# Kernel optimization log

Measured on AMD Instinct MI355X. Metric: run time of the kernel, lower is better.

## Reference

```python
import jax, jax.numpy as jnp
import numpy as np

B, N, C = 8, 1024, 768
H, D = 12, 64  # num_heads, head_dim
SCALE = D ** -0.5


def setup_inputs() -> dict:
    key = jax.random.key(0)
    ks = jax.random.split(key, 6)
    x = jax.random.normal(ks[0], (B, N, C), dtype=jnp.float32)
    # per-head Linear weights stacked: [H, D, C] (torch Linear stores [out, in])
    Wq = jax.random.normal(ks[1], (H, D, C), dtype=jnp.float32) * 0.02
    Wk = jax.random.normal(ks[2], (H, D, C), dtype=jnp.float32) * 0.02
    Wv = jax.random.normal(ks[3], (H, D, C), dtype=jnp.float32) * 0.02
    Wp = jax.random.normal(ks[4], (C, C), dtype=jnp.float32) * 0.02
    bp = jnp.zeros((C,), dtype=jnp.float32)
    return {"x": x, "Wq": Wq, "Wk": Wk, "Wv": Wv, "Wp": Wp, "bp": bp}


def reference(x, Wq, Wk, Wv, Wp, bp):
    # Per-head projections (batched across heads): [B, H, N, D]
    q = jnp.einsum('bnc,hdc->bhnd', x, Wq) * SCALE
    k = jnp.einsum('bnc,hdc->bhnd', x, Wk)
    v = jnp.einsum('bnc,hdc->bhnd', x, Wv)
    # Scaled dot-product attention per head
    attn = jax.nn.softmax(jnp.einsum('bhnd,bhmd->bhnm', q, k), axis=-1)
    out = jnp.einsum('bhnm,bhmd->bhnd', attn, v)
    # Concat heads along last dim == transpose to [B, N, H, D] then reshape
    out = out.transpose(0, 2, 1, 3).reshape(x.shape[0], x.shape[1], -1)
    # Output projection
    return out @ Wp.T + bp
```

## Files before the change

### kernel.cpp

```cpp
#include <hip/hip_runtime.h>

typedef unsigned short u16;
typedef __attribute__((ext_vector_type(8))) __bf16 bf16x8;
typedef __attribute__((ext_vector_type(4))) float f32x4;

__device__ __forceinline__ u16 f2bf(float f) {
    union { float f; unsigned u; } v; v.f = f;
    unsigned u = v.u;
    u += 0x7FFFu + ((u >> 16) & 1u);
    return (u16)(u >> 16);
}

typedef const __attribute__((address_space(1))) void GV;
typedef __attribute__((address_space(3))) void LV;
__device__ __forceinline__ void gl2lds16(const void* g, void* l) {
    __builtin_amdgcn_global_load_lds((GV*)g, (LV*)l, 16, 0, 0);
}

__global__ void cast_f32_to_bf16(const float* __restrict__ in, u16* __restrict__ out, int n4) {
    int i = blockIdx.x * 256 + threadIdx.x;
    if (i < n4) {
        float4 f = reinterpret_cast<const float4*>(in)[i];
        ushort4 o;
        o.x = f2bf(f.x); o.y = f2bf(f.y); o.z = f2bf(f.z); o.w = f2bf(f.w);
        reinterpret_cast<ushort4*>(out)[i] = o;
    }
}

__device__ __forceinline__ void stage_tile32(const u16* src, int k0, u16* lds, int tid) {
    #pragma unroll
    for (int half = 0; half < 2; half++) {
        int i = half * 256 + tid;
        int row = i >> 2, p = i & 3;
        int l = (p - (row >> 1)) & 3;
        gl2lds16(src + (size_t)row * 768 + k0 + l * 8, lds + i * 8);
    }
}
__device__ __forceinline__ const bf16x8* frag32(const u16* lds, int row, int quad) {
    return reinterpret_cast<const bf16x8*>(lds + row * 32 + (((quad + (row >> 1)) & 3) * 8));
}

__global__ __launch_bounds__(256, 2) void gemm_qkv(
    const u16* __restrict__ A, const u16* __restrict__ Bm,
    u16* __restrict__ qo, u16* __restrict__ ko, u16* __restrict__ vto)
{
    __shared__ u16 As[4096];
    __shared__ u16 Bs[4096];
    const int tid = threadIdx.x;
    const int wave = tid >> 6, lane = tid & 63;
    const int quad = lane >> 4, l16 = lane & 15;
    const int wr = (wave >> 1) * 64, wc = (wave & 1) * 64;
    const int rowBase = blockIdx.y * 128;
    const int colBase = blockIdx.x * 128;

    f32x4 acc[4][4] = {};
    const u16* aSrc = A + (size_t)rowBase * 768;
    const u16* bSrc = Bm + (size_t)colBase * 768;

    for (int k0 = 0; k0 < 768; k0 += 32) {
        __syncthreads();
        stage_tile32(aSrc, k0, As, tid);
        stage_tile32(bSrc, k0, Bs, tid);
        __syncthreads();
        bf16x8 a[4], b[4];
        #pragma unroll
        for (int mi = 0; mi < 4; mi++)
            a[mi] = *frag32(As, wr + mi * 16 + l16, quad);
        #pragma unroll
        for (int ni = 0; ni < 4; ni++)
            b[ni] = *frag32(Bs, wc + ni * 16 + l16, quad);
        #pragma unroll
        for (int mi = 0; mi < 4; mi++)
            #pragma unroll
            for (int ni = 0; ni < 4; ni++)
                acc[mi][ni] = __builtin_amdgcn_mfma_f32_16x16x32_bf16(a[mi], b[ni], acc[mi][ni], 0, 0, 0);
    }

    #pragma unroll
    for (int mi = 0; mi < 4; mi++) {
        #pragma unroll
        for (int ni = 0; ni < 4; ni++) {
            int gj = colBase + wc + ni * 16 + l16;
            int which = gj / 768;
            int r = gj - which * 768;
            int h = r >> 6, d = r & 63;
            int gi0 = rowBase + wr + mi * 16 + quad * 4;
            int b_ = gi0 >> 10;
            int n0 = gi0 & 1023;
            if (which == 2) {
                ushort4 pk;
                pk.x = f2bf(acc[mi][ni][0]);
                pk.y = f2bf(acc[mi][ni][1]);
                pk.z = f2bf(acc[mi][ni][2]);
                pk.w = f2bf(acc[mi][ni][3]);
                *reinterpret_cast<ushort4*>(vto + ((size_t)(b_ * 12 + h) * 64 + d) * 1024 + n0) = pk;
            } else {
                float s = (which == 0) ? 0.125f : 1.0f;
                u16* dst = (which == 0 ? qo : ko) + ((size_t)(b_ * 12 + h) * 1024 + n0) * 64 + d;
                #pragma unroll
                for (int rr = 0; rr < 4; rr++)
                    dst[(size_t)rr * 64] = f2bf(acc[mi][ni][rr] * s);
            }
        }
    }
}

__global__ __launch_bounds__(256, 3) void attn_fwd(
    const u16* __restrict__ q, const u16* __restrict__ k,
    const u16* __restrict__ vt, u16* __restrict__ ao)
{
    __shared__ u16 Ks[2][4096];
    __shared__ u16 Vs[2][4096];
    __shared__ u16 Ps[128][72];
    const int bh = blockIdx.x, qt = blockIdx.y;
    const int b = bh / 12, h = bh - b * 12;
    const int tid = threadIdx.x;
    const int wave = tid >> 6, lane = tid & 63;
    const int quad = lane >> 4, l16 = lane & 15;
    const int swz = l16 & 7;
    u16 (*PsW)[72] = &Ps[wave * 32];

    const u16* qb = q + (size_t)bh * 65536 + ((size_t)qt * 128 + wave * 32) * 64;
    const u16* kb = k + (size_t)bh * 65536;
    const u16* vb = vt + (size_t)bh * 65536;

    auto stage = [&](int buf, int j0) {
        #pragma unroll
        for (int r = 0; r < 2; r++) {
            int i = r * 256 + tid;
            int row = i >> 3, cp = i & 7;
            int cl = cp ^ (row & 7);
            gl2lds16((const char*)kb + (size_t)(j0 + row) * 128 + cl * 16,
                     (char*)&Ks[buf][0] + i * 16);
        }
        #pragma unroll
        for (int r = 0; r < 2; r++) {
            int i = r * 256 + tid;
            int row = i >> 3, cp = i & 7;
            int cl = cp ^ (row & 7);
            gl2lds16((const char*)vb + (size_t)row * 2048 + (size_t)j0 * 2 + cl * 16,
                     (char*)&Vs[buf][0] + i * 16);
        }
    };

    stage(0, 0);

    bf16x8 qf[2][2];
    #pragma unroll
    for (int ni = 0; ni < 2; ni++)
        #pragma unroll
        for (int ks = 0; ks < 2; ks++)
            qf[ni][ks] = *reinterpret_cast<const bf16x8*>(qb + (ni * 16 + l16) * 64 + ks * 32 + quad * 8);

    f32x4 o[2][4] = {};
    float lsum[2] = {0.f, 0.f};

    __syncthreads();

    int buf = 0;
    for (int j0 = 0; j0 < 1024; j0 += 64) {
        if (j0 + 64 < 1024) stage(buf ^ 1, j0 + 64);

        f32x4 s[4][2] = {};
        #pragma unroll
        for (int ks = 0; ks < 2; ks++) {
            bf16x8 kf[4];
            #pragma unroll
            for (int mi = 0; mi < 4; mi++) {
                int row = mi * 16 + l16;
                int ch = (ks * 4 + quad) ^ swz;
                kf[mi] = *reinterpret_cast<const bf16x8*>(&Ks[buf][row * 64 + ch * 8]);
            }
            #pragma unroll
            for (int mi = 0; mi < 4; mi++)
                #pragma unroll
                for (int ni = 0; ni < 2; ni++)
                    s[mi][ni] = __builtin_amdgcn_mfma_f32_16x16x32_bf16(kf[mi], qf[ni][ks], s[mi][ni], 0, 0, 0);
        }

        #pragma unroll
        for (int mi = 0; mi < 4; mi++) {
            #pragma unroll
            for (int ni = 0; ni < 2; ni++) {
                float p0 = __expf(s[mi][ni][0]);
                float p1 = __expf(s[mi][ni][1]);
                float p2 = __expf(s[mi][ni][2]);
                float p3 = __expf(s[mi][ni][3]);
                lsum[ni] += (p0 + p1) + (p2 + p3);
                ushort4 pk;
                pk.x = f2bf(p0); pk.y = f2bf(p1); pk.z = f2bf(p2); pk.w = f2bf(p3);
                *reinterpret_cast<ushort4*>(&PsW[ni * 16 + l16][mi * 16 + quad * 4]) = pk;
            }
        }

        #pragma unroll
        for (int ks = 0; ks < 2; ks++) {
            bf16x8 vf[4], pf[2];
            #pragma unroll
            for (int di = 0; di < 4; di++) {
                int row = di * 16 + l16;
                int ch = (ks * 4 + quad) ^ swz;
                vf[di] = *reinterpret_cast<const bf16x8*>(&Vs[buf][row * 64 + ch * 8]);
            }
            #pragma unroll
            for (int mi = 0; mi < 2; mi++)
                pf[mi] = *reinterpret_cast<const bf16x8*>(&PsW[mi * 16 + l16][ks * 32 + quad * 8]);
            #pragma unroll
            for (int mi = 0; mi < 2; mi++)
                #pragma unroll
                for (int di = 0; di < 4; di++)
                    o[mi][di] = __builtin_amdgcn_mfma_f32_16x16x32_bf16(pf[mi], vf[di], o[mi][di], 0, 0, 0);
        }

        __syncthreads();
        buf ^= 1;
    }

    #pragma unroll
    for (int ni = 0; ni < 2; ni++) {
        lsum[ni] += __shfl_xor(lsum[ni], 16, 64);
        lsum[ni] += __shfl_xor(lsum[ni], 32, 64);
    }

    #pragma unroll
    for (int mi = 0; mi < 2; mi++) {
        #pragma unroll
        for (int r = 0; r < 4; r++) {
            float lv = __shfl(lsum[mi], quad * 4 + r, 16);
            float inv = 1.0f / lv;
            int n = qt * 128 + wave * 32 + mi * 16 + quad * 4 + r;
            size_t base = (size_t)(b * 1024 + n) * 768 + h * 64;
            #pragma unroll
            for (int di = 0; di < 4; di++)
                ao[base + di * 16 + l16] = f2bf(o[mi][di][r] * inv);
        }
    }
}

__global__ __launch_bounds__(256, 2) void gemm_proj(
    const u16* __restrict__ A, const u16* __restrict__ Bm,
    const float* __restrict__ bias, float* __restrict__ out)
{
    __shared__ u16 As[4096];
    __shared__ u16 Bs[4096];
    const int tid = threadIdx.x;
    const int wave = tid >> 6, lane = tid & 63;
    const int quad = lane >> 4, l16 = lane & 15;
    const int wr = (wave >> 1) * 64, wc = (wave & 1) * 64;
    const int rowBase = blockIdx.y * 128;
    const int colBase = blockIdx.x * 128;

    f32x4 acc[4][4] = {};
    const u16* aSrc = A + (size_t)rowBase * 768;
    const u16* bSrc = Bm + (size_t)colBase * 768;

    for (int k0 = 0; k0 < 768; k0 += 32) {
        __syncthreads();
        stage_tile32(aSrc, k0, As, tid);
        stage_tile32(bSrc, k0, Bs, tid);
        __syncthreads();
        bf16x8 a[4], b[4];
        #pragma unroll
        for (int mi = 0; mi < 4; mi++)
            a[mi] = *frag32(As, wr + mi * 16 + l16, quad);
        #pragma unroll
        for (int ni = 0; ni < 4; ni++)
            b[ni] = *frag32(Bs, wc + ni * 16 + l16, quad);
        #pragma unroll
        for (int mi = 0; mi < 4; mi++)
            #pragma unroll
            for (int ni = 0; ni < 4; ni++)
                acc[mi][ni] = __builtin_amdgcn_mfma_f32_16x16x32_bf16(a[mi], b[ni], acc[mi][ni], 0, 0, 0);
    }

    #pragma unroll
    for (int mi = 0; mi < 4; mi++) {
        #pragma unroll
        for (int ni = 0; ni < 4; ni++) {
            int gj = colBase + wc + ni * 16 + l16;
            float bv = bias[gj];
            int gi0 = rowBase + wr + mi * 16 + quad * 4;
            #pragma unroll
            for (int rr2 = 0; rr2 < 4; rr2++)
                out[(size_t)(gi0 + rr2) * 768 + gj] = acc[mi][ni][rr2] + bv;
        }
    }
}

extern "C" void kernel_launch(void* const* d_in, const int* in_sizes, int n_in,
                              void* d_out, int out_size, void* d_ws, size_t ws_size,
                              hipStream_t stream) {
    const float* x  = (const float*)d_in[0];
    const float* Wq = (const float*)d_in[1];
    const float* Wk = (const float*)d_in[2];
    const float* Wv = (const float*)d_in[3];
    const float* Wp = (const float*)d_in[4];
    const float* bp = (const float*)d_in[5];
    float* out = (float*)d_out;

    u16* xb  = (u16*)d_ws;
    u16* wb  = xb  + 6291456;
    u16* wpb = wb  + 1769472;
    u16* qo  = wpb + 589824;
    u16* ko  = qo  + 6291456;
    u16* vto = ko  + 6291456;
    u16* ao  = vto + 6291456;

    cast_f32_to_bf16<<<6144, 256, 0, stream>>>(x,  xb,  1572864);
    cast_f32_to_bf16<<<576,  256, 0, stream>>>(Wq, wb,            147456);
    cast_f32_to_bf16<<<576,  256, 0, stream>>>(Wk, wb + 589824,   147456);
    cast_f32_to_bf16<<<576,  256, 0, stream>>>(Wv, wb + 1179648,  147456);
    cast_f32_to_bf16<<<576,  256, 0, stream>>>(Wp, wpb,           147456);

    gemm_qkv<<<dim3(18, 64), 256, 0, stream>>>(xb, wb, qo, ko, vto);
    attn_fwd<<<dim3(96, 8), 256, 0, stream>>>(qo, ko, vto, ao);
    gemm_proj<<<dim3(6, 64), 256, 0, stream>>>(ao, wpb, bp, out);
}
```

Before: 207.3 us.

## Double-buffer LDS tiles in GEMMs and fuse five cast launches into one

Both the QKV and output-projection GEMMs now keep two LDS buffers and issue the global-to-LDS load for the next K tile before the MFMA work on the current one. This cuts the loop from two barriers per iteration to one, so load latency can overlap compute. Separately, the five f32-to-bf16 cast launches are merged into one kernel that picks its source and destination from the block index, removing launch overhead. LDS use per block doubles to 32 KB, which could limit occupancy. It also relies on the global_load_lds writes having completed by the time of the single barrier.

Result: faster. 195.7 us (-5.6%).

```diff
diff --git a/kernel.cpp b/kernel.cpp
--- a/kernel.cpp
+++ b/kernel.cpp
@@ -17,14 +17,27 @@
     __builtin_amdgcn_global_load_lds((GV*)g, (LV*)l, 16, 0, 0);
 }
 
-__global__ void cast_f32_to_bf16(const float* __restrict__ in, u16* __restrict__ out, int n4) {
-    int i = blockIdx.x * 256 + threadIdx.x;
-    if (i < n4) {
-        float4 f = reinterpret_cast<const float4*>(in)[i];
-        ushort4 o;
-        o.x = f2bf(f.x); o.y = f2bf(f.y); o.z = f2bf(f.z); o.w = f2bf(f.w);
-        reinterpret_cast<ushort4*>(out)[i] = o;
-    }
+__global__ __launch_bounds__(256) void cast_all(
+    const float* __restrict__ x,  const float* __restrict__ Wq,
+    const float* __restrict__ Wk, const float* __restrict__ Wv,
+    const float* __restrict__ Wp,
+    u16* __restrict__ xb, u16* __restrict__ wb, u16* __restrict__ wpb)
+{
+    int bid = blockIdx.x;
+    const float4* s; ushort4* d; int idx;
+    if (bid < 6144) {
+        s = (const float4*)x; d = (ushort4*)xb; idx = bid * 256 + threadIdx.x;
+    } else {
+        int t = bid - 6144;
+        int w = t / 576;
+        idx = (t - w * 576) * 256 + threadIdx.x;
+        s = (const float4*)(w == 0 ? Wq : w == 1 ? Wk : w == 2 ? Wv : Wp);
+        d = (ushort4*)(w == 3 ? wpb : wb + w * 589824);
+    }
+    float4 f = s[idx];
+    ushort4 o;
+    o.x = f2bf(f.x); o.y = f2bf(f.y); o.z = f2bf(f.z); o.w = f2bf(f.w);
+    d[idx] = o;
 }
 
 __device__ __forceinline__ void stage_tile32(const u16* src, int k0, u16* lds, int tid) {
@@ -44,8 +57,8 @@
     const u16* __restrict__ A, const u16* __restrict__ Bm,
     u16* __restrict__ qo, u16* __restrict__ ko, u16* __restrict__ vto)
 {
-    __shared__ u16 As[4096];
-    __shared__ u16 Bs[4096];
+    __shared__ u16 As[2][4096];
+    __shared__ u16 Bs[2][4096];
     const int tid = threadIdx.x;
     const int wave = tid >> 6, lane = tid & 63;
     const int quad = lane >> 4, l16 = lane & 15;
@@ -57,23 +70,30 @@
     const u16* aSrc = A + (size_t)rowBase * 768;
     const u16* bSrc = Bm + (size_t)colBase * 768;
 
+    stage_tile32(aSrc, 0, As[0], tid);
+    stage_tile32(bSrc, 0, Bs[0], tid);
+    __syncthreads();
+
+    int buf = 0;
     for (int k0 = 0; k0 < 768; k0 += 32) {
-        __syncthreads();
-        stage_tile32(aSrc, k0, As, tid);
-        stage_tile32(bSrc, k0, Bs, tid);
-        __syncthreads();
+        if (k0 + 32 < 768) {
+            stage_tile32(aSrc, k0 + 32, As[buf ^ 1], tid);
+            stage_tile32(bSrc, k0 + 32, Bs[buf ^ 1], tid);
+        }
         bf16x8 a[4], b[4];
         #pragma unroll
         for (int mi = 0; mi < 4; mi++)
-            a[mi] = *frag32(As, wr + mi * 16 + l16, quad);
+            a[mi] = *frag32(As[buf], wr + mi * 16 + l16, quad);
         #pragma unroll
         for (int ni = 0; ni < 4; ni++)
-            b[ni] = *frag32(Bs, wc + ni * 16 + l16, quad);
+            b[ni] = *frag32(Bs[buf], wc + ni * 16 + l16, quad);
         #pragma unroll
         for (int mi = 0; mi < 4; mi++)
             #pragma unroll
             for (int ni = 0; ni < 4; ni++)
                 acc[mi][ni] = __builtin_amdgcn_mfma_f32_16x16x32_bf16(a[mi], b[ni], acc[mi][ni], 0, 0, 0);
+        __syncthreads();
+        buf ^= 1;
     }
 
     #pragma unroll
@@ -241,8 +261,8 @@
     const u16* __restrict__ A, const u16* __restrict__ Bm,
     const float* __restrict__ bias, float* __restrict__ out)
 {
-    __shared__ u16 As[4096];
-    __shared__ u16 Bs[4096];
+    __shared__ u16 As[2][4096];
+    __shared__ u16 Bs[2][4096];
     const int tid = threadIdx.x;
     const int wave = tid >> 6, lane = tid & 63;
     const int quad = lane >> 4, l16 = lane & 15;
@@ -254,23 +274,30 @@
     const u16* aSrc = A + (size_t)rowBase * 768;
     const u16* bSrc = Bm + (size_t)colBase * 768;
 
+    stage_tile32(aSrc, 0, As[0], tid);
+    stage_tile32(bSrc, 0, Bs[0], tid);
+    __syncthreads();
+
+    int buf = 0;
     for (int k0 = 0; k0 < 768; k0 += 32) {
-        __syncthreads();
-        stage_tile32(aSrc, k0, As, tid);
-        stage_tile32(bSrc, k0, Bs, tid);
-        __syncthreads();
+        if (k0 + 32 < 768) {
+            stage_tile32(aSrc, k0 + 32, As[buf ^ 1], tid);
+            stage_tile32(bSrc, k0 + 32, Bs[buf ^ 1], tid);
+        }
         bf16x8 a[4], b[4];
         #pragma unroll
         for (int mi = 0; mi < 4; mi++)
-            a[mi] = *frag32(As, wr + mi * 16 + l16, quad);
+            a[mi] = *frag32(As[buf], wr + mi * 16 + l16, quad);
         #pragma unroll
         for (int ni = 0; ni < 4; ni++)
-            b[ni] = *frag32(Bs, wc + ni * 16 + l16, quad);
+            b[ni] = *frag32(Bs[buf], wc + ni * 16 + l16, quad);
         #pragma unroll
         for (int mi = 0; mi < 4; mi++)
             #pragma unroll
             for (int ni = 0; ni < 4; ni++)
                 acc[mi][ni] = __builtin_amdgcn_mfma_f32_16x16x32_bf16(a[mi], b[ni], acc[mi][ni], 0, 0, 0);
+        __syncthreads();
+        buf ^= 1;
     }
 
     #pragma unroll
@@ -306,12 +333,7 @@
     u16* vto = ko  + 6291456;
     u16* ao  = vto + 6291456;
 
-    cast_f32_to_bf16<<<6144, 256, 0, stream>>>(x,  xb,  1572864);
-    cast_f32_to_bf16<<<576,  256, 0, stream>>>(Wq, wb,            147456);
-    cast_f32_to_bf16<<<576,  256, 0, stream>>>(Wk, wb + 589824,   147456);
-    cast_f32_to_bf16<<<576,  256, 0, stream>>>(Wv, wb + 1179648,  147456);
-    cast_f32_to_bf16<<<576,  256, 0, stream>>>(Wp, wpb,           147456);
-
+    cast_all<<<8448, 256, 0, stream>>>(x, Wq, Wk, Wv, Wp, xb, wb, wpb);
     gemm_qkv<<<dim3(18, 64), 256, 0, stream>>>(xb, wb, qo, ko, vto);
     attn_fwd<<<dim3(96, 8), 256, 0, stream>>>(qo, ko, vto, ao);
     gemm_proj<<<dim3(6, 64), 256, 0, stream>>>(ao, wpb, bp, out);
```
